# Kernel tuning notes

Hardware: AMD Instinct MI355X
Metric: run time of the kernel (lower is better)

Reference implementation:

```python
import jax, jax.numpy as jnp
import numpy as np

B, I, T, H, K = 64, 32, 1024, 512, 8  # K = number of extra pathways


def setup_inputs() -> dict:
    key = jax.random.key(0)
    ks = jax.random.split(key, 32)
    stdv = 1.0 / np.sqrt(H)
    u = lambda k, shp: jax.random.uniform(k, shp, jnp.float32, -stdv, stdv)
    inp = {}
    inp['Y'] = jax.random.normal(ks[0], (B, I, T), jnp.float32)
    for j in range(K):
        inp[f'x{j+1}'] = jax.random.normal(ks[1 + j], (B, 3, T), jnp.float32)
    # main gates
    inp['W_i'], inp['U_i'], inp['b_i'] = u(ks[9], (I, H)), u(ks[10], (H, H)), u(ks[11], (H,))
    inp['W_f'], inp['U_f'], inp['b_f'] = u(ks[12], (I, H)), u(ks[13], (H, H)), u(ks[14], (H,))
    inp['W_c'], inp['U_c'], inp['b_c'] = u(ks[15], (I, H)), u(ks[16], (H, H)), u(ks[17], (H,))
    inp['W_o'], inp['U_o'], inp['b_o'] = u(ks[18], (I, H)), u(ks[19], (H, H)), u(ks[20], (H,))
    # stacked extra pathways: [K,3,H], [K,H,H], [K,H]
    inp['W_i_x'] = u(ks[21], (K, 3, H))
    inp['U_i_x'] = u(ks[22], (K, H, H))
    inp['b_i_x'] = u(ks[23], (K, H))
    inp['W_c_x'] = u(ks[24], (K, 3, H))
    inp['U_c_x'] = u(ks[25], (K, H, H))
    inp['b_c_x'] = u(ks[26], (K, H))
    inp['W_a'], inp['b_a'] = u(ks[27], (H, H)), u(ks[28], (H,))
    return inp


def _forward(Y, x1, x2, x3, x4, x5, x6, x7, x8,
             W_i, U_i, b_i, W_f, U_f, b_f, W_c, U_c, b_c, W_o, U_o, b_o,
             W_i_x, U_i_x, b_i_x, W_c_x, U_c_x, b_c_x, W_a, b_a):
    xs = jnp.stack([x1, x2, x3, x4, x5, x6, x7, x8], axis=0)  # [K,B,3,T]
    # Original code quirk: input gates i_x3..i_x8 all consume x2_t.
    gate_idx = jnp.array([0, 1, 1, 1, 1, 1, 1, 1])
    xs_i = xs[gate_idx]                                        # [K,B,3,T]
    Y_T = jnp.transpose(Y, (2, 0, 1))        # [T,B,I]
    xsi_T = jnp.transpose(xs_i, (3, 1, 0, 2))  # [T,B,K,3]
    xsc_T = jnp.transpose(xs, (3, 1, 0, 2))    # [T,B,K,3]

    def step(carry, inp):
        h, c = carry
        Y_t, xi_t, xc_t = inp
        i_t = jax.nn.sigmoid(Y_t @ W_i + h @ U_i + b_i)                      # [B,H]
        i_x = jax.nn.sigmoid(jnp.einsum('bki,kih->bkh', xi_t, W_i_x)
                             + jnp.einsum('bh,kho->bko', h, U_i_x) + b_i_x)  # [B,K,H]
        f_t = jax.nn.sigmoid(Y_t @ W_f + h @ U_f + b_f)
        Ct = jnp.tanh(Y_t @ W_c + h @ U_c + b_c)
        Cx = jnp.tanh(jnp.einsum('bki,kih->bkh', xc_t, W_c_x)
                      + jnp.einsum('bh,kho->bko', h, U_c_x) + b_c_x)
        o_t = jax.nn.sigmoid(Y_t @ W_o + h @ U_o + b_o)
        l_all = jnp.concatenate([(Ct * i_t)[:, None, :], Cx * i_x], axis=1)  # [B,9,H]
        u_all = jnp.tanh(jnp.einsum('bkh,ho->bko', l_all, W_a) * c[:, None, :] + b_a)
        alpha = jax.nn.softmax(u_all, axis=1)
        L_t = jnp.sum(alpha * l_all, axis=1)                                 # [B,H]
        c = f_t * c + L_t
        h = o_t * jnp.tanh(c)
        return (h, c), h

    h0 = jnp.zeros((Y.shape[0], W_a.shape[0]), Y.dtype)
    (h_T, _), hs = jax.lax.scan(step, (h0, h0), (Y_T, xsi_T, xsc_T))
    hidden_seq = jnp.transpose(hs, (1, 0, 2))  # [B,T,H]
    return h_T, hidden_seq


def reference(Y, x1, x2, x3, x4, x5, x6, x7, x8,
              W_i, U_i, b_i, W_f, U_f, b_f, W_c, U_c, b_c, W_o, U_o, b_o,
              W_i_x, U_i_x, b_i_x, W_c_x, U_c_x, b_c_x, W_a, b_a):
    return _forward(Y, x1, x2, x3, x4, x5, x6, x7, x8,
                    W_i, U_i, b_i, W_f, U_f, b_f, W_c, U_c, b_c, W_o, U_o, b_o,
                    W_i_x, U_i_x, b_i_x, W_c_x, U_c_x, b_c_x, W_a, b_a)
```

## Files before the change

### kernel.cpp

```cpp
#include <hip/hip_runtime.h>
#include <hip/hip_bf16.h>

typedef __hip_bfloat16 bf16;
typedef unsigned long long u64;

#define NSTEP 1024
#define BATCH 64
#define HID   512
#define GRID  256
#define NTHR  512
#define KC    64

#define OFF_BAR   0u
#define OFF_FLAG  64u
#define OFF_HG    256u
#define OFF_CG    131328u
#define OFF_GALL  262400u
#define OFF_UCAT  2883840u
#define OFF_WA    23855360u
#define OFF_WM    24903936u
#define OFF_WX    25166080u
#define OFF_BM    25362688u
#define OFF_BX    25370880u
#define OFF_BA    25403648u
#define OFF_YT    25405696u
#define OFF_XT    33794304u

#define L_US    0
#define L_WML   20960
#define L_HA    22400
#define L_YA    31104
#define L_XA    33216
#define L_RED   34752
#define L_GB    31104
#define L_LB    31104
#define L_MP    35784
#define L_TOT   39240

#define US(c,k)    smem[L_US  + (c)*524 + (k)]
#define WML(c,j)   smem[L_WML + (c)*36  + (j)]
#define HA(s,b,k)  smem[L_HA  + (s)*4352 + (b)*68 + (k)]
#define YA(b,j)    smem[L_YA  + (b)*33 + (j)]
#define XA(a,b,j)  smem[L_XA  + ((a)*64 + (b))*3 + (j)]
#define RED(q,j)   smem[L_RED + (q)*11 + (j)]
#define GB(r,c)    smem[L_GB  + (r)*40 + (c)]
#define LB(j,h)    smem[L_LB  + (j)*520 + (h)]
#define MP(q,j)    smem[L_MP  + (q)*27 + (j)]

struct RawIn {
  const void *Y, *x[8];
  const void *W_i,*U_i,*b_i, *W_f,*U_f,*b_f, *W_c,*U_c,*b_c, *W_o,*U_o,*b_o;
  const void *W_ix,*U_ix,*b_ix, *W_cx,*U_cx,*b_cx, *W_a,*b_a;
  float *Ucat,*Wa,*Wm,*Wx,*Bm,*Bx,*Ba,*Yt,*Xt;
  const unsigned *flag;
};

struct Params {
  const float *Ucat,*Wa,*Wm,*Wx,*Bm,*Bx,*Ba,*Yt,*Xt;
  float *Hg,*Cg,*Gall;
  unsigned *bar;
  const unsigned *flag;
  void *out;
};

__global__ void k_detect(const unsigned short* __restrict__ p, unsigned* flag) {
  if (blockIdx.x == 0 && threadIdx.x == 0) {
    int cnt = 0;
    for (int i = 0; i < 64; ++i) {
      unsigned e = (p[i] >> 7) & 0xFF;
      cnt += (e >= 0x60 && e <= 0x7C) || (p[i] & 0x7FFF) == 0;
    }
    *flag = (cnt >= 56) ? 1u : 0u;
  }
}

__device__ __forceinline__ float cvt(const void* p, size_t i, bool bf) {
  return bf ? (float)((const bf16*)p)[i] : ((const float*)p)[i];
}

#define NWTOT 5605888
__global__ __launch_bounds__(256)
void k_conv_w(RawIn R) {
  const bool bf = (*R.flag) != 0;
  for (size_t i = blockIdx.x*256 + threadIdx.x; i < NWTOT; i += (size_t)gridDim.x*256) {
    if (i < 5242880) {
      size_t g = i >> 18, r = i & 262143;
      const void* s = g<4 ? (g==0?R.U_i:g==1?R.U_f:g==2?R.U_c:R.U_o)
                    : g<12 ? R.U_ix : R.U_cx;
      size_t off = g<4 ? r : g<12 ? (g-4)*262144 + r : (g-12)*262144 + r;
      R.Ucat[i] = cvt(s, off, bf);
    } else {
      size_t j = i - 5242880;
      if (j < 262144) { R.Wa[j] = cvt(R.W_a, j, bf); }
      else {
        size_t j2 = j - 262144;
        if (j2 < 65536) {
          size_t g = j2 >> 14, r = j2 & 16383;
          const void* s = g==0?R.W_i:g==1?R.W_f:g==2?R.W_c:R.W_o;
          R.Wm[j2] = cvt(s, r, bf);
        } else {
          size_t j3 = j2 - 65536;
          if (j3 < 24576) {
            size_t p = j3 / 1536, r = j3 % 1536;
            R.Wx[j3] = p < 8 ? cvt(R.W_ix, p*1536 + r, bf)
                             : cvt(R.W_cx, (p-8)*1536 + r, bf);
          } else {
            size_t j4 = j3 - 24576;
            if (j4 < 2048) {
              size_t g = j4 >> 9, c = j4 & 511;
              const void* s = g==0?R.b_i:g==1?R.b_f:g==2?R.b_c:R.b_o;
              R.Bm[j4] = cvt(s, c, bf);
            } else {
              size_t j5 = j4 - 2048;
              if (j5 < 8192) {
                size_t p = j5 >> 9, c = j5 & 511;
                R.Bx[j5] = p < 8 ? cvt(R.b_ix, p*512 + c, bf)
                                 : cvt(R.b_cx, (p-8)*512 + c, bf);
              } else {
                size_t j6 = j5 - 8192;
                R.Ba[j6] = cvt(R.b_a, j6, bf);
              }
            }
          }
        }
      }
    }
  }
}

#define NYT 2097152
#define NXT 1572864
__global__ __launch_bounds__(256)
void k_conv_in(RawIn R) {
  const bool bf = (*R.flag) != 0;
  for (size_t i = blockIdx.x*256 + threadIdx.x; i < NYT+NXT; i += (size_t)gridDim.x*256) {
    if (i < NYT) {
      size_t j = i & 31, b = (i >> 5) & 63, t = i >> 11;
      R.Yt[i] = cvt(R.Y, (b*32 + j)*NSTEP + t, bf);
    } else {
      size_t i2 = i - NYT;
      size_t j = i2 % 3, r = i2 / 3;
      size_t b = r & 63; r >>= 6;
      size_t a = r & 7, t = r >> 3;
      R.Xt[i2] = cvt(R.x[a], (b*3 + j)*NSTEP + t, bf);
    }
  }
}


__device__ __forceinline__ float sigf(float v){ return 1.f/(1.f+expf(-v)); }

__device__ __forceinline__ float gload(const float* p){
  return __hip_atomic_load(p, __ATOMIC_RELAXED, __HIP_MEMORY_SCOPE_AGENT);
}
__device__ __forceinline__ u64 gload2(const float* p){
  return __hip_atomic_load((const u64*)p, __ATOMIC_RELAXED, __HIP_MEMORY_SCOPE_AGENT);
}
__device__ __forceinline__ void gstore(float* p, float v){
  __hip_atomic_store(p, v, __ATOMIC_RELAXED, __HIP_MEMORY_SCOPE_AGENT);
}
__device__ __forceinline__ void gstore2(float* p, float x, float y){
  union { u64 u_; float f[2]; } v; v.f[0]=x; v.f[1]=y;
  __hip_atomic_store((u64*)p, v.u_, __ATOMIC_RELAXED, __HIP_MEMORY_SCOPE_AGENT);
}

__device__ __forceinline__ void gbar(unsigned* bar, unsigned bi) {
  asm volatile("s_waitcnt vmcnt(0)" ::: "memory");
  __syncthreads();
  if (threadIdx.x == 0) {
    __hip_atomic_fetch_add(bar, 1u, __ATOMIC_RELAXED, __HIP_MEMORY_SCOPE_AGENT);
    unsigned* rel = bar + 32;
    if (blockIdx.x == 0) {
      while (__hip_atomic_load(bar, __ATOMIC_RELAXED, __HIP_MEMORY_SCOPE_AGENT) < bi*GRID)
        __builtin_amdgcn_s_sleep(1);
      __hip_atomic_store(rel, bi, __ATOMIC_RELAXED, __HIP_MEMORY_SCOPE_AGENT);
    } else {
      while (__hip_atomic_load(rel, __ATOMIC_RELAXED, __HIP_MEMORY_SCOPE_AGENT) < bi)
        __builtin_amdgcn_s_sleep(2);
    }
  }
  __syncthreads();
}


__global__ __launch_bounds__(NTHR)
void lstm_main(Params P) {
  extern __shared__ float smem[];

  const bool bfout = (*P.flag) != 0;

  const int w   = blockIdx.x;
  const int tid = threadIdx.x;
  const int c0  = w * 40;
  const int cgr = tid & 7;
  const int rgr = (tid >> 3) & 31;
  const int ksl = tid >> 8;
  const int cl  = cgr * 5;
  const int pb  = w >> 2;
  const int ph0 = (w & 3) * 128;
  const int hl  = tid & 127;
  const int kq  = tid >> 7;
  const int hp  = ph0 + hl;

  for (int e = tid; e < 40*512; e += NTHR) {
    int c = e >> 9, k = e & 511;
    int cg = c0 + c, g = cg >> 9, cc = cg & 511;
    US(c, k) = P.Ucat[((size_t)g*HID + k)*HID + cc];
  }
  for (int e = tid; e < 40*33; e += NTHR) {
    int c = e / 33, jj = e % 33;
    int cg = c0 + c, g = cg >> 9, cc = cg & 511;
    float v;
    if (jj == 32) {
      v = g < 4  ? P.Bm[g*HID + cc]
        : g < 12 ? P.Bx[(g-4)*HID + cc]
                 : P.Bx[(8 + g-12)*HID + cc];
    } else if (g < 4) {
      v = P.Wm[((size_t)g*32 + jj)*HID + cc];
    } else if (jj < 3) {
      int p = (g < 12) ? (g-4) : (8 + g-12);
      v = P.Wx[((size_t)p*3 + jj)*HID + cc];
    } else v = 0.f;
    WML(c, jj) = v;
  }
  __syncthreads();

  unsigned bi = 0;

  u64 pre[8];
  auto hgld = [&](int kcc) {
#pragma unroll
    for (int u = 0; u < 8; ++u) {
      int e2 = tid + u*NTHR;
      int s2 = e2 >> 11, b = (e2 >> 5) & 63, k = (e2 & 31) * 2;
      pre[u] = gload2(&P.Hg[(size_t)b*HID + s2*256 + kcc + k]);
    }
  };

  for (int t = 0; t < NSTEP; ++t) {
    for (int e = tid; e < 64*32; e += NTHR) {
      int b = e >> 5, j = e & 31;
      YA(b, j) = P.Yt[((size_t)t*BATCH + b)*32 + j];
    }
    for (int e = tid; e < 8*64*3; e += NTHR) {
      int j2 = e % 3; int r = e / 3; int b = r & 63; int a = r >> 6;
      XA(a, b, j2) = P.Xt[(((size_t)t*8 + a)*BATCH + b)*3 + j2];
    }

    hgld(0);

    float acc[2][5];
#pragma unroll
    for (int i=0;i<2;++i)
#pragma unroll
      for (int j=0;j<5;++j) acc[i][j]=0.f;

    for (int kc = 0; kc < 256; kc += KC) {
      __syncthreads();
#pragma unroll
      for (int u = 0; u < 8; ++u) {
        int e2 = tid + u*NTHR;
        int s2 = e2 >> 11, b = (e2 >> 5) & 63, k = (e2 & 31) * 2;
        union { u64 u_; float f[2]; } v; v.u_ = pre[u];
        float2 t2; t2.x = v.f[0]; t2.y = v.f[1];
        *(float2*)&HA(s2, b, k) = t2;
      }
      __syncthreads();
      if (kc + KC < 256) hgld(kc + KC);

      const int kb = ksl*256 + kc;
#pragma unroll 4
      for (int kk = 0; kk < KC; kk += 4) {
        float4 h0 = *(const float4*)&HA(ksl, rgr,      kk);
        float4 h1 = *(const float4*)&HA(ksl, rgr+32,   kk);
#pragma unroll
        for (int j = 0; j < 5; ++j) {
          float4 u = *(const float4*)&US(cl+j, kb+kk);
          acc[0][j] += h0.x*u.x; acc[0][j] += h0.y*u.y;
          acc[0][j] += h0.z*u.z; acc[0][j] += h0.w*u.w;
          acc[1][j] += h1.x*u.x; acc[1][j] += h1.y*u.y;
          acc[1][j] += h1.z*u.z; acc[1][j] += h1.w*u.w;
        }
      }
    }

    if (ksl) {
      int q = tid - 256;
#pragma unroll
      for (int i=0;i<2;++i)
#pragma unroll
        for (int j=0;j<5;++j) RED(q, i*5+j) = acc[i][j];
    }
    __syncthreads();

    float vv[2][5];
    if (!ksl) {
#pragma unroll
      for (int i = 0; i < 2; ++i) {
        int row = rgr + 32*i;
#pragma unroll
        for (int j = 0; j < 5; ++j) {
          int c = cl + j, cg = c0 + c, g = cg >> 9;
          float v = acc[i][j] + RED(tid, i*5+j);
          float s = WML(c, 32);
          if (g < 4) {
            for (int jj = 0; jj < 32; ++jj)
              s += YA(row, jj) * WML(c, jj);
            v += s;
            v = (g==2) ? tanhf(v) : sigf(v);
          } else if (g < 12) {
            int p = g-4; int a = (p==0) ? 0 : 1;
            for (int jj = 0; jj < 3; ++jj)
              s += XA(a, row, jj) * WML(c, jj);
            v = sigf(v + s);
          } else {
            int p = g-12;
            for (int jj = 0; jj < 3; ++jj)
              s += XA(p, row, jj) * WML(c, jj);
            v = tanhf(v + s);
          }
          vv[i][j] = v;
        }
      }
    }
    __syncthreads();
    if (!ksl) {
#pragma unroll
      for (int i = 0; i < 2; ++i)
#pragma unroll
        for (int j = 0; j < 5; ++j)
          GB(rgr + 32*i, cl + j) = vv[i][j];
    }
    __syncthreads();
    for (int e = tid; e < 64*20; e += NTHR) {
      int row = e / 20, p = e % 20;
      int cc2 = c0 + 2*p;
      int g = cc2 >> 9, cc = cc2 & 511;
      gstore2(&P.Gall[((size_t)g*BATCH + row)*HID + cc], GB(row, 2*p), GB(row, 2*p+1));
    }

    gbar(P.bar, ++bi);

    for (int e = tid; e < 9*256; e += NTHR) {
      int j = e >> 8, h2 = (e & 255) << 1;
      union { u64 u_; float f[2]; } a, b2;
      if (j == 0) {
        a.u_  = gload2(&P.Gall[((size_t)0*BATCH+pb)*HID+h2]);
        b2.u_ = gload2(&P.Gall[((size_t)2*BATCH+pb)*HID+h2]);
      } else {
        int p = j-1;
        a.u_  = gload2(&P.Gall[((size_t)(4+p)*BATCH+pb)*HID+h2]);
        b2.u_ = gload2(&P.Gall[((size_t)(12+p)*BATCH+pb)*HID+h2]);
      }
      float2 t2; t2.x = a.f[0]*b2.f[0]; t2.y = a.f[1]*b2.f[1];
      *(float2*)&LB(j, h2) = t2;
    }
    __syncthreads();

    float a9[9];
#pragma unroll
    for (int j=0;j<9;++j) a9[j]=0.f;
    {
      const int k0 = kq * 128;
      const float* wa = P.Wa + (size_t)k0*HID + hp;
#pragma unroll 2
      for (int k = 0; k < 128; k += 4) {
        float w0 = wa[(size_t)(k+0)*HID];
        float w1 = wa[(size_t)(k+1)*HID];
        float w2 = wa[(size_t)(k+2)*HID];
        float w3 = wa[(size_t)(k+3)*HID];
#pragma unroll
        for (int j=0;j<9;++j) {
          float4 l4 = *(const float4*)&LB(j, k0+k);
          a9[j] += l4.x*w0; a9[j] += l4.y*w1; a9[j] += l4.z*w2; a9[j] += l4.w*w3;
        }
      }
    }
    if (kq) {
#pragma unroll
      for (int j=0;j<9;++j) MP(hl, (kq-1)*9 + j) = a9[j];
    }
    __syncthreads();
    if (!kq) {
      float co = P.Cg[(size_t)pb*HID + hp];
      float ba = P.Ba[hp];
      float u9[9], mx = -1e30f;
#pragma unroll
      for (int j=0;j<9;++j) {
        float m = a9[j] + MP(hl, j) + MP(hl, 9+j) + MP(hl, 18+j);
        u9[j] = tanhf(m*co + ba);
        mx = fmaxf(mx, u9[j]);
      }
      float ssum = 0.f, L = 0.f;
#pragma unroll
      for (int j=0;j<9;++j) {
        float e2 = expf(u9[j]-mx);
        ssum += e2;
        L += e2 * LB(j, hp);
      }
      L /= ssum;
      float f = gload(&P.Gall[((size_t)1*BATCH+pb)*HID + hp]);
      float o = gload(&P.Gall[((size_t)3*BATCH+pb)*HID + hp]);
      float cn = f*co + L;
      float hn = o*tanhf(cn);
      P.Cg[(size_t)pb*HID + hp] = cn;
      gstore(&P.Hg[(size_t)pb*HID + hp], hn);
      size_t iseq = (size_t)BATCH*HID + ((size_t)pb*NSTEP + t)*HID + hp;
      if (bfout) ((bf16*)P.out)[iseq] = __float2bfloat16(hn);
      else       ((float*)P.out)[iseq] = hn;
      if (t == NSTEP-1) {
        size_t ih = (size_t)pb*HID + hp;
        if (bfout) ((bf16*)P.out)[ih] = __float2bfloat16(hn);
        else       ((float*)P.out)[ih] = hn;
      }
    }

    gbar(P.bar, ++bi);
  }
}


extern "C" void kernel_launch(void* const* d_in, const int* in_sizes, int n_in,
                              void* d_out, int out_size, void* d_ws, size_t ws_size,
                              hipStream_t stream) {
  char* ws = (char*)d_ws;

  RawIn R;
  R.Y = d_in[0];
  for (int i = 0; i < 8; ++i) R.x[i] = d_in[1+i];
  R.W_i=d_in[9];  R.U_i=d_in[10]; R.b_i=d_in[11];
  R.W_f=d_in[12]; R.U_f=d_in[13]; R.b_f=d_in[14];
  R.W_c=d_in[15]; R.U_c=d_in[16]; R.b_c=d_in[17];
  R.W_o=d_in[18]; R.U_o=d_in[19]; R.b_o=d_in[20];
  R.W_ix=d_in[21]; R.U_ix=d_in[22]; R.b_ix=d_in[23];
  R.W_cx=d_in[24]; R.U_cx=d_in[25]; R.b_cx=d_in[26];
  R.W_a =d_in[27]; R.b_a =d_in[28];
  R.Ucat=(float*)(ws+OFF_UCAT); R.Wa=(float*)(ws+OFF_WA);
  R.Wm=(float*)(ws+OFF_WM); R.Wx=(float*)(ws+OFF_WX);
  R.Bm=(float*)(ws+OFF_BM); R.Bx=(float*)(ws+OFF_BX); R.Ba=(float*)(ws+OFF_BA);
  R.Yt=(float*)(ws+OFF_YT); R.Xt=(float*)(ws+OFF_XT);
  R.flag=(const unsigned*)(ws+OFF_FLAG);

  Params P;
  P.Ucat=R.Ucat; P.Wa=R.Wa; P.Wm=R.Wm; P.Wx=R.Wx;
  P.Bm=R.Bm; P.Bx=R.Bx; P.Ba=R.Ba; P.Yt=R.Yt; P.Xt=R.Xt;
  P.Hg=(float*)(ws+OFF_HG); P.Cg=(float*)(ws+OFF_CG); P.Gall=(float*)(ws+OFF_GALL);
  P.bar=(unsigned*)(ws+OFF_BAR);
  P.flag=R.flag;
  P.out=d_out;

  hipMemsetAsync(d_ws, 0, OFF_GALL, stream);

  k_detect<<<1, 64, 0, stream>>>((const unsigned short*)d_in[10], (unsigned*)(ws+OFF_FLAG));
  k_conv_w <<<21899, 256, 0, stream>>>(R);
  k_conv_in<<<14336, 256, 0, stream>>>(R);

  const int smemBytes = L_TOT * 4;
  hipFuncSetAttribute((const void*)lstm_main,
                      hipFuncAttributeMaxDynamicSharedMemorySize, smemBytes);
  lstm_main<<<dim3(GRID), dim3(NTHR), smemBytes, stream>>>(P);
}
```

Measured before the change: 61.55 ms.

## Use hierarchical per-XCD grid barrier and retile attention matvec with tree reduction

New measurement: 51.85 ms. 15.8% less time.

```diff
diff --git a/kernel.cpp b/kernel.cpp
--- a/kernel.cpp
+++ b/kernel.cpp
@@ -12,19 +12,19 @@
 #define KC    64
 
 #define OFF_BAR   0u
-#define OFF_FLAG  64u
-#define OFF_HG    256u
-#define OFF_CG    131328u
-#define OFF_GALL  262400u
-#define OFF_UCAT  2883840u
-#define OFF_WA    23855360u
-#define OFF_WM    24903936u
-#define OFF_WX    25166080u
-#define OFF_BM    25362688u
-#define OFF_BX    25370880u
-#define OFF_BA    25403648u
-#define OFF_YT    25405696u
-#define OFF_XT    33794304u
+#define OFF_FLAG  640u
+#define OFF_HG    1024u
+#define OFF_CG    132096u
+#define OFF_GALL  263168u
+#define OFF_UCAT  2884608u
+#define OFF_WA    23856128u
+#define OFF_WM    24904704u
+#define OFF_WX    25166848u
+#define OFF_BM    25265152u
+#define OFF_BX    25273344u
+#define OFF_BA    25306112u
+#define OFF_YT    25308160u
+#define OFF_XT    33696768u
 
 #define L_US    0
 #define L_WML   20960
@@ -32,9 +32,11 @@
 #define L_YA    31104
 #define L_XA    33216
 #define L_RED   34752
-#define L_GB    31104
+#define L_GB    36224
 #define L_LB    31104
-#define L_MP    35784
+#define L_RA    22400
+#define L_RB    27264
+#define L_MPZ   29696
 #define L_TOT   39240
 
 #define US(c,k)    smem[L_US  + (c)*524 + (k)]
@@ -45,7 +47,6 @@
 #define RED(q,j)   smem[L_RED + (q)*11 + (j)]
 #define GB(r,c)    smem[L_GB  + (r)*40 + (c)]
 #define LB(j,h)    smem[L_LB  + (j)*520 + (h)]
-#define MP(q,j)    smem[L_MP  + (q)*27 + (j)]
 
 struct RawIn {
   const void *Y, *x[8];
@@ -164,14 +165,22 @@
   __hip_atomic_store((u64*)p, v.u_, __ATOMIC_RELAXED, __HIP_MEMORY_SCOPE_AGENT);
 }
 
-__device__ __forceinline__ void gbar(unsigned* bar, unsigned bi) {
+__device__ __forceinline__ void gbar(unsigned* base, unsigned bi, int w) {
   asm volatile("s_waitcnt vmcnt(0)" ::: "memory");
   __syncthreads();
   if (threadIdx.x == 0) {
-    __hip_atomic_fetch_add(bar, 1u, __ATOMIC_RELAXED, __HIP_MEMORY_SCOPE_AGENT);
-    unsigned* rel = bar + 32;
-    if (blockIdx.x == 0) {
-      while (__hip_atomic_load(bar, __ATOMIC_RELAXED, __HIP_MEMORY_SCOPE_AGENT) < bi*GRID)
+    unsigned* xcd  = base + 16 + 16*(w & 7);
+    unsigned* glob = base;
+    unsigned* rel  = base + 144;
+    __hip_atomic_fetch_add(xcd, 1u, __ATOMIC_RELAXED, __HIP_MEMORY_SCOPE_AGENT);
+    if (w < 8) {
+      unsigned* mine = base + 16 + 16*w;
+      while (__hip_atomic_load(mine, __ATOMIC_RELAXED, __HIP_MEMORY_SCOPE_AGENT) < bi*32u)
+        __builtin_amdgcn_s_sleep(1);
+      __hip_atomic_fetch_add(glob, 1u, __ATOMIC_RELAXED, __HIP_MEMORY_SCOPE_AGENT);
+    }
+    if (w == 0) {
+      while (__hip_atomic_load(glob, __ATOMIC_RELAXED, __HIP_MEMORY_SCOPE_AGENT) < bi*8u)
         __builtin_amdgcn_s_sleep(1);
       __hip_atomic_store(rel, bi, __ATOMIC_RELAXED, __HIP_MEMORY_SCOPE_AGENT);
     } else {
@@ -183,7 +192,7 @@
 }
 
 
-__global__ __launch_bounds__(NTHR)
+__global__ __launch_bounds__(NTHR, 2)
 void lstm_main(Params P) {
   extern __shared__ float smem[];
 
@@ -198,9 +207,8 @@
   const int cl  = cgr * 5;
   const int pb  = w >> 2;
   const int ph0 = (w & 3) * 128;
-  const int hl  = tid & 127;
-  const int kq  = tid >> 7;
-  const int hp  = ph0 + hl;
+  const int hg  = tid & 63;
+  const int kq8 = tid >> 6;
 
   for (int e = tid; e < 40*512; e += NTHR) {
     int c = e >> 9, k = e & 511;
@@ -339,7 +347,7 @@
       gstore2(&P.Gall[((size_t)g*BATCH + row)*HID + cc], GB(row, 2*p), GB(row, 2*p+1));
     }
 
-    gbar(P.bar, ++bi);
+    gbar(P.bar, ++bi, w);
 
     for (int e = tid; e < 9*256; e += NTHR) {
       int j = e >> 8, h2 = (e & 255) << 1;
@@ -357,38 +365,86 @@
     }
     __syncthreads();
 
-    float a9[9];
-#pragma unroll
-    for (int j=0;j<9;++j) a9[j]=0.f;
+    float ab[2][9];
+#pragma unroll
+    for (int s=0;s<2;++s)
+#pragma unroll
+      for (int j=0;j<9;++j) ab[s][j]=0.f;
     {
-      const int k0 = kq * 128;
-      const float* wa = P.Wa + (size_t)k0*HID + hp;
-#pragma unroll 2
-      for (int k = 0; k < 128; k += 4) {
-        float w0 = wa[(size_t)(k+0)*HID];
-        float w1 = wa[(size_t)(k+1)*HID];
-        float w2 = wa[(size_t)(k+2)*HID];
-        float w3 = wa[(size_t)(k+3)*HID];
+      const int k0 = kq8 * 64;
+      const float* wa = P.Wa + (size_t)k0*HID + ph0 + hg*2;
+#pragma unroll 4
+      for (int k = 0; k < 64; k += 4) {
+        float2 w0 = *(const float2*)&wa[(size_t)(k+0)*HID];
+        float2 w1 = *(const float2*)&wa[(size_t)(k+1)*HID];
+        float2 w2 = *(const float2*)&wa[(size_t)(k+2)*HID];
+        float2 w3 = *(const float2*)&wa[(size_t)(k+3)*HID];
 #pragma unroll
         for (int j=0;j<9;++j) {
           float4 l4 = *(const float4*)&LB(j, k0+k);
-          a9[j] += l4.x*w0; a9[j] += l4.y*w1; a9[j] += l4.z*w2; a9[j] += l4.w*w3;
+          ab[0][j] += l4.x*w0.x; ab[0][j] += l4.y*w1.x;
+          ab[0][j] += l4.z*w2.x; ab[0][j] += l4.w*w3.x;
+          ab[1][j] += l4.x*w0.y; ab[1][j] += l4.y*w1.y;
+          ab[1][j] += l4.z*w2.y; ab[1][j] += l4.w*w3.y;
         }
       }
     }
-    if (kq) {
-#pragma unroll
-      for (int j=0;j<9;++j) MP(hl, (kq-1)*9 + j) = a9[j];
-    }
-    __syncthreads();
-    if (!kq) {
+    if (tid >= 256) {
+      float* r = &smem[L_RA + (tid-256)*19];
+#pragma unroll
+      for (int s=0;s<2;++s)
+#pragma unroll
+        for (int j=0;j<9;++j) r[s*9+j] = ab[s][j];
+    }
+    __syncthreads();
+    if (tid < 256) {
+      const float* r = &smem[L_RA + tid*19];
+#pragma unroll
+      for (int s=0;s<2;++s)
+#pragma unroll
+        for (int j=0;j<9;++j) ab[s][j] += r[s*9+j];
+      if (tid >= 128) {
+        float* r2 = &smem[L_RB + (tid-128)*19];
+#pragma unroll
+        for (int s=0;s<2;++s)
+#pragma unroll
+          for (int j=0;j<9;++j) r2[s*9+j] = ab[s][j];
+      }
+    }
+    __syncthreads();
+    if (tid < 128) {
+      const float* r = &smem[L_RB + tid*19];
+#pragma unroll
+      for (int s=0;s<2;++s)
+#pragma unroll
+        for (int j=0;j<9;++j) ab[s][j] += r[s*9+j];
+      if (tid >= 64) {
+        float* r2 = &smem[L_RA + (tid-64)*19];
+#pragma unroll
+        for (int s=0;s<2;++s)
+#pragma unroll
+          for (int j=0;j<9;++j) r2[s*9+j] = ab[s][j];
+      }
+    }
+    __syncthreads();
+    if (tid < 64) {
+      const float* r = &smem[L_RA + tid*19];
+      float* mp = &smem[L_MPZ + tid*19];
+#pragma unroll
+      for (int s=0;s<2;++s)
+#pragma unroll
+        for (int j=0;j<9;++j) mp[s*9+j] = ab[s][j] + r[s*9+j];
+    }
+    __syncthreads();
+    if (tid < 128) {
+      const int hp = ph0 + tid;
+      const float* mf = &smem[L_MPZ + (tid>>1)*19 + (tid&1)*9];
       float co = P.Cg[(size_t)pb*HID + hp];
       float ba = P.Ba[hp];
       float u9[9], mx = -1e30f;
 #pragma unroll
       for (int j=0;j<9;++j) {
-        float m = a9[j] + MP(hl, j) + MP(hl, 9+j) + MP(hl, 18+j);
-        u9[j] = tanhf(m*co + ba);
+        u9[j] = tanhf(mf[j]*co + ba);
         mx = fmaxf(mx, u9[j]);
       }
       float ssum = 0.f, L = 0.f;
@@ -415,7 +471,7 @@
       }
     }
 
-    gbar(P.bar, ++bi);
+    gbar(P.bar, ++bi, w);
   }
 }
 
```
